# Kernel optimization log

Measured on AMD Instinct MI355X. Metric: run time of the kernel, lower is better.

The kernel has to match this reference:

```python
import jax, jax.numpy as jnp
import numpy as np

B, N, E = 4, 2048, 1024
A, H = 64, 16          # attention_feature_dim, heads
D = A                   # per-head dim per source's rearrange quirk: d = attention_feature_dim
DK = A / H              # source scales by sqrt(attention_feature_dim / heads) = sqrt(4)
NEG_INF = jnp.float32(-jnp.inf)


def setup_inputs() -> dict:
    key = jax.random.key(0)
    ks = jax.random.split(key, 6)
    x = jax.random.normal(ks[0], (B, N, E), dtype=jnp.float32)
    mask = jax.random.randint(ks[1], (B, N), 0, 2, dtype=jnp.int32)
    # nn.Linear(E, A*H*3): weight [out,in] -> store transposed [in,out] for x @ W
    w_qkv = jax.random.normal(ks[2], (E, A * H * 3), dtype=jnp.float32) / np.sqrt(E)
    b_qkv = jax.random.normal(ks[3], (A * H * 3,), dtype=jnp.float32) * 0.02
    w_out = jax.random.normal(ks[4], (A * H, E), dtype=jnp.float32) / np.sqrt(A * H)
    b_out = jax.random.normal(ks[5], (E,), dtype=jnp.float32) * 0.02
    return {"x": x, "mask": mask, "w_qkv": w_qkv, "b_qkv": b_qkv,
            "w_out": w_out, "b_out": b_out}


def reference(x, mask, w_qkv, b_qkv, w_out, b_out):
    b, n, _ = x.shape
    qkv = x @ w_qkv + b_qkv                         # [b, n, 3*H*D]
    q, k, v = jnp.split(qkv, 3, axis=-1)            # each [b, n, H*D]
    def to_heads(t):
        return t.reshape(b, n, H, D).transpose(0, 2, 1, 3)  # [b, H, n, D]
    q, k, v = to_heads(q), to_heads(k), to_heads(v)
    scale = jnp.float32(1.0 / np.sqrt(DK))
    scores = jnp.einsum('bhqd,bhkd->bhqk', q, k) * scale    # [b, H, n, n]
    # mask: [b, n] -> [b, 1, 1, n]; masked positions (==0) get -inf
    scores = jnp.where(mask[:, None, None, :] == 0, NEG_INF, scores)
    attn = jax.nn.softmax(scores, axis=-1)
    out = jnp.einsum('bhqk,bhkd->bhqd', attn, v)            # [b, H, n, D]
    out = out.transpose(0, 2, 1, 3).reshape(b, n, H * D)    # [b, n, H*D]
    return out @ w_out + b_out                              # [b, n, E]
```

## Files before the change

kernel.cpp:

```cpp
#include <hip/hip_runtime.h>


typedef __bf16 bf16;
typedef __attribute__((ext_vector_type(8))) __bf16 bf16x8;
typedef __attribute__((ext_vector_type(4))) float f32x4;

#define MFMA16(a, b, c) __builtin_amdgcn_mfma_f32_16x16x32_bf16(a, b, c, 0, 0, 0)
#define GLOAD_LDS(src, dst) __builtin_amdgcn_global_load_lds( \
    (const __attribute__((address_space(1))) void*)(src),     \
    (__attribute__((address_space(3))) void*)(dst), 16, 0, 0)
#define BAR() __builtin_amdgcn_s_barrier()
#define VMCNT(n) asm volatile("s_waitcnt vmcnt(" #n ")" ::: "memory")

#define QSCALE 0.72134752f

__device__ __forceinline__ void transpose_tile(
    const float* __restrict__ in, bf16* __restrict__ out, int R, int C,
    int scale_rows, float scale, int bx, int by, int t, float (*s)[65])
{
    const int r0 = by * 64;
    const int c0 = bx * 64;
    const int tr  = t >> 4;
    const int tc4 = (t & 15) * 4;
#pragma unroll
    for (int p = 0; p < 4; ++p) {
        int r = tr + p * 16;
        float4 v = *(const float4*)(in + (size_t)(r0 + r) * C + c0 + tc4);
        s[r][tc4 + 0] = v.x; s[r][tc4 + 1] = v.y;
        s[r][tc4 + 2] = v.z; s[r][tc4 + 3] = v.w;
    }
    __syncthreads();
    const int cw  = t >> 3;
    const int rw8 = (t & 7) * 8;
#pragma unroll
    for (int p = 0; p < 2; ++p) {
        int c = cw + p * 32;
        float f = (c0 + c) < scale_rows ? scale : 1.0f;
        union { uint4 v; bf16 h[8]; } u;
#pragma unroll
        for (int j = 0; j < 8; ++j) u.h[j] = (bf16)(s[rw8 + j][c] * f);
        *(uint4*)(out + (size_t)(c0 + c) * R + r0 + rw8) = u.v;
    }
}

__global__ __launch_bounds__(256, 1) void prep_kernel(
    const float* __restrict__ x, bf16* __restrict__ xb,
    const float* __restrict__ w_qkv, bf16* __restrict__ wqkvT,
    const float* __restrict__ w_out, bf16* __restrict__ woutT)
{
    __shared__ float s[64][65];
    const int t = threadIdx.x;
    int blk = blockIdx.x;
    if (blk < 8192) {
        int i = blk * 256 + t;
        float4 v = *(const float4*)(x + (size_t)i * 4);
        union { ushort4 u; bf16 h[4]; } o;
        o.h[0] = (bf16)v.x; o.h[1] = (bf16)v.y;
        o.h[2] = (bf16)v.z; o.h[3] = (bf16)v.w;
        *(ushort4*)(xb + (size_t)i * 4) = o.u;
        return;
    }
    blk -= 8192;
    if (blk < 768) {
        transpose_tile(w_qkv, wqkvT, 1024, 3072, 1024, QSCALE,
                       blk % 48, blk / 48, t, s);
    } else {
        blk -= 768;
        transpose_tile(w_out, woutT, 1024, 1024, 0, 1.0f,
                       blk % 16, blk / 16, t, s);
    }
}

template <typename OutT>
__global__ __launch_bounds__(512, 2) void gemm128x256_kernel(
    const bf16* __restrict__ A, const bf16* __restrict__ Bt,
    const float* __restrict__ bias, OutT* __restrict__ C,
    int M, int ldc, int K, int qcols, float qscale, int nbx,
    bf16* __restrict__ vtg)
{
    __shared__ __align__(16) bf16 As[3 * 128 * 64];
    __shared__ __align__(16) bf16 Bs[3 * 256 * 64];

    const int t    = threadIdx.x;
    const int lane = t & 63;
    const int wave = t >> 6;
    const int wr   = wave >> 2;
    const int wc   = wave & 3;
    const int l15  = lane & 15;
    const int g    = lane >> 4;

    const int nwg  = gridDim.x;
    const int per  = nwg >> 3;
    const int mper = per / nbx;
    const int wg   = blockIdx.x;
    const int xcd  = wg & 7;
    const int idx  = wg >> 3;
    const int m0   = (xcd * mper + idx % mper) * 128;
    const int n0   = (idx / mper) * 256;

    const int ntile = K >> 6;

    int srow[2], sblk[2];
#pragma unroll
    for (int r = 0; r < 2; ++r) {
        int s = t * 16 + r * 8192;
        srow[r] = s >> 7;
        int blk = (s >> 4) & 7;
        sblk[r] = blk ^ (srow[r] & 7);
    }
    const int ldst0 = t * 8;

    const bf16* Abase = A  + (size_t)m0 * K;
    const bf16* Bbase = Bt + (size_t)n0 * K;

    const f32x4 z = {0.f, 0.f, 0.f, 0.f};
    f32x4 acc[4][4];
#pragma unroll
    for (int i = 0; i < 4; ++i)
#pragma unroll
        for (int j = 0; j < 4; ++j) acc[i][j] = z;

    auto stageA = [&](int tile, int slot) {
        if (tile >= ntile) return;
        bf16* dst = As + slot * 8192;
        const bf16* src = Abase + tile * 64;
#pragma unroll
        for (int r = 0; r < 2; ++r)
            GLOAD_LDS(src + (size_t)srow[r] * K + sblk[r] * 8,
                      dst + ldst0 + r * 4096);
    };
    auto stageBh = [&](int tile, int slot, int h) {
        if (tile >= ntile) return;
        bf16* dst = Bs + slot * 16384 + h * 8192;
        const bf16* src = Bbase + (size_t)(h * 128) * K + tile * 64;
#pragma unroll
        for (int r = 0; r < 2; ++r)
            GLOAD_LDS(src + (size_t)srow[r] * K + sblk[r] * 8,
                      dst + ldst0 + r * 4096);
    };

#define LOAD_AF(slot)                                                         \
    _Pragma("unroll")                                                         \
    for (int f = 0; f < 4; ++f) {                                             \
        int row = wr * 64 + f * 16 + l15;                                     \
        _Pragma("unroll")                                                     \
        for (int ks = 0; ks < 2; ++ks)                                        \
            af[f][ks] = *(const bf16x8*)(&As[(slot) * 8192 + row * 64 +       \
                            (((ks * 4 + g) ^ (row & 7)) * 8)]);               \
    }
#define LOAD_BF(slot, half, dstv)                                             \
    _Pragma("unroll")                                                         \
    for (int c2 = 0; c2 < 2; ++c2) {                                          \
        int row = wc * 64 + ((half) * 2 + c2) * 16 + l15;                     \
        _Pragma("unroll")                                                     \
        for (int ks = 0; ks < 2; ++ks)                                        \
            dstv[c2][ks] = *(const bf16x8*)(&Bs[(slot) * 16384 + row * 64 +   \
                            (((ks * 4 + g) ^ (row & 7)) * 8)]);               \
    }
#define MFMA_H(bv, half)                                                      \
    {                                                                         \
        __builtin_amdgcn_s_setprio(1);                                        \
        _Pragma("unroll")                                                     \
        for (int f = 0; f < 4; ++f)                                           \
            _Pragma("unroll")                                                 \
            for (int c2 = 0; c2 < 2; ++c2) {                                  \
                acc[f][(half) * 2 + c2] = MFMA16(                             \
                    af[f][0], bv[c2][0], acc[f][(half) * 2 + c2]);            \
                acc[f][(half) * 2 + c2] = MFMA16(                             \
                    af[f][1], bv[c2][1], acc[f][(half) * 2 + c2]);            \
            }                                                                 \
        __builtin_amdgcn_s_setprio(0);                                        \
    }

    stageA(0, 0); stageBh(0, 0, 0); stageBh(0, 0, 1);
    stageA(1, 1); stageBh(1, 1, 0); stageBh(1, 1, 1);
    VMCNT(6);
    BAR();

    int slot = 0;
    for (int T = 0; T < ntile; ++T) {
        int slot2 = slot + 2; if (slot2 >= 3) slot2 -= 3;
        bf16x8 af[4][2], blo[2][2], bhi[2][2];
        LOAD_AF(slot);
        LOAD_BF(slot, 0, blo);
        stageA(T + 2, slot2);
        stageBh(T + 2, slot2, 0);
        MFMA_H(blo, 0);
        BAR();
        LOAD_BF(slot, 1, bhi);
        stageBh(T + 2, slot2, 1);
        MFMA_H(bhi, 1);
        if (T + 1 < ntile) {
            if (T + 2 < ntile) { VMCNT(6); } else { VMCNT(0); }
        }
        BAR();
        slot = (slot == 2) ? 0 : slot + 1;
    }

#undef LOAD_AF
#undef LOAD_BF
#undef MFMA_H

    if (vtg != nullptr && n0 >= 2048) {
        const int b = m0 >> 11;
#pragma unroll
        for (int f = 0; f < 4; ++f) {
            int row = m0 + wr * 64 + f * 16 + g * 4;
            int n   = row & 2047;
#pragma unroll
            for (int cf = 0; cf < 4; ++cf) {
                int col = n0 + wc * 64 + cf * 16 + l15;
                int c2  = col - 2048;
                int h   = c2 >> 6;
                int d   = c2 & 63;
                float bs = bias[col];
                union { bf16 hh[4]; ushort4 u; } s;
#pragma unroll
                for (int r = 0; r < 4; ++r)
                    s.hh[r] = (bf16)(acc[f][cf][r] + bs);
                *(ushort4*)(vtg + (size_t)(b * 16 + h) * 131072 +
                            (size_t)d * 2048 + n) = s.u;
            }
        }
    } else {
#pragma unroll
        for (int f = 0; f < 4; ++f) {
            int row = m0 + wr * 64 + f * 16 + g * 4;
#pragma unroll
            for (int cf = 0; cf < 4; ++cf) {
                int col = n0 + wc * 64 + cf * 16 + l15;
                float bs = bias[col];
                if (col < qcols) bs *= qscale;
#pragma unroll
                for (int r = 0; r < 4; ++r) {
                    float v = acc[f][cf][r] + bs;
                    C[(size_t)(row + r) * ldc + col] = (OutT)v;
                }
            }
        }
    }
}

__global__ __launch_bounds__(256, 3) void attn_kernel(
    const bf16* __restrict__ qkv, const bf16* __restrict__ vtg,
    const int* __restrict__ mask, bf16* __restrict__ O)
{
    __shared__ __align__(16) bf16 Ks[2][64 * 64];
    __shared__ __align__(16) bf16 Vt[2][64 * 64];
    __shared__ __align__(16) bf16 Ps[4][16 * 88];
    __shared__ __align__(16) float mneg[2048];

    const int t    = threadIdx.x;
    const int lane = t & 63;
    const int wave = t >> 6;
    const int l15  = lane & 15;
    const int g    = lane >> 4;

    const int bid = (blockIdx.x & 7) * 128 + (blockIdx.x >> 3);
    const int qt  = bid & 15;
    const int bh  = bid >> 4;
    const int h   = bh & 15;
    const int b   = bh >> 4;
    const int q0  = qt * 128 + wave * 16;

    const int* mrow = mask + b * 2048;
    for (int i = t; i < 2048; i += 256)
        mneg[i] = mrow[i] ? 0.0f : -1e30f;

    const size_t RS = 2048;
    const bf16* qp0 = qkv + (size_t)(b * 2048 + q0 + l15) * RS + h * 64 + g * 8;
    const bf16* qp1 = qp0 + (size_t)64 * RS;
    bf16x8 aQ[2][2];
    aQ[0][0] = *(const bf16x8*)(qp0);
    aQ[0][1] = *(const bf16x8*)(qp0 + 32);
    aQ[1][0] = *(const bf16x8*)(qp1);
    aQ[1][1] = *(const bf16x8*)(qp1 + 32);

    const bf16* kbase = qkv + (size_t)(b * 2048) * RS + 1024 + h * 64;
    const bf16* vbase = vtg + (size_t)bh * (64 * 2048);

    const int e0 = t * 8;
    int srow[2], scol[2];
#pragma unroll
    for (int r = 0; r < 2; ++r) {
        int e   = e0 + r * 2048;
        int row = e >> 6;
        int cb  = (e >> 3) & 7;
        srow[r] = row;
        scol[r] = ((cb ^ (row & 7)) * 8);
    }

    const int rb0 = ((g)     ^ (l15 & 7)) * 8;
    const int rb1 = ((4 + g) ^ (l15 & 7)) * 8;

    const f32x4 z = {0.f, 0.f, 0.f, 0.f};
    f32x4 o0[4] = {z, z, z, z}, o1[4] = {z, z, z, z};
    f32x4 lacc0 = z, lacc1 = z;

    bf16x8 ones;
#pragma unroll
    for (int j = 0; j < 8; ++j) ones[j] = (bf16)1.0f;

#pragma unroll
    for (int r = 0; r < 2; ++r) {
        GLOAD_LDS(kbase + (size_t)srow[r] * RS + scol[r],   &Ks[0][e0 + r * 2048]);
        GLOAD_LDS(vbase + (size_t)srow[r] * 2048 + scol[r], &Vt[0][e0 + r * 2048]);
    }
    asm volatile("s_waitcnt vmcnt(0)" ::: "memory");
    __syncthreads();

    for (int i = 0; i < 32; ++i) {
        const int kc  = i * 64;
        const int buf = i & 1;

        if (i + 1 < 32) {
#pragma unroll
            for (int r = 0; r < 2; ++r) {
                GLOAD_LDS(kbase + (size_t)(kc + 64 + srow[r]) * RS + scol[r],
                          &Ks[buf ^ 1][e0 + r * 2048]);
                GLOAD_LDS(vbase + (size_t)srow[r] * 2048 + kc + 64 + scol[r],
                          &Vt[buf ^ 1][e0 + r * 2048]);
            }
        }

        f32x4 mb4[4];
#pragma unroll
        for (int kt = 0; kt < 4; ++kt)
#pragma unroll
            for (int r = 0; r < 4; ++r)
                mb4[kt][r] = mneg[kc + kt * 16 + g * 4 + r];

        bf16x8 bk[4][2];
#pragma unroll
        for (int kt = 0; kt < 4; ++kt) {
            const bf16* kr = &Ks[buf][(kt * 16 + l15) * 64];
            bk[kt][0] = *(const bf16x8*)(kr + rb0);
            bk[kt][1] = *(const bf16x8*)(kr + rb1);
        }

        f32x4 S[4];
#pragma unroll
        for (int kt = 0; kt < 4; ++kt) {
            S[kt] = MFMA16(bk[kt][0], aQ[0][0], mb4[kt]);
            S[kt] = MFMA16(bk[kt][1], aQ[0][1], S[kt]);
        }
#pragma unroll
        for (int kt = 0; kt < 4; ++kt) {
            union { bf16 hh[4]; ushort4 u; } pk;
#pragma unroll
            for (int r = 0; r < 4; ++r)
                pk.hh[r] = (bf16)__builtin_amdgcn_exp2f(S[kt][r]);
            *(ushort4*)(&Ps[wave][l15 * 88 + kt * 16 + g * 4]) = pk.u;
        }
        asm volatile("s_waitcnt lgkmcnt(0)" ::: "memory");
        __builtin_amdgcn_sched_barrier(0);
        const bf16x8 aP00 = *(const bf16x8*)(&Ps[wave][l15 * 88 + g * 8]);
        const bf16x8 aP01 = *(const bf16x8*)(&Ps[wave][l15 * 88 + 32 + g * 8]);
        asm volatile("s_waitcnt lgkmcnt(0)" ::: "memory");
        __builtin_amdgcn_sched_barrier(0);

#pragma unroll
        for (int kt = 0; kt < 4; ++kt) {
            S[kt] = MFMA16(bk[kt][0], aQ[1][0], mb4[kt]);
            S[kt] = MFMA16(bk[kt][1], aQ[1][1], S[kt]);
        }

        bf16x8 bv[4][2];
#pragma unroll
        for (int dt = 0; dt < 4; ++dt) {
            const bf16* vr = &Vt[buf][(dt * 16 + l15) * 64];
            bv[dt][0] = *(const bf16x8*)(vr + rb0);
            bv[dt][1] = *(const bf16x8*)(vr + rb1);
        }

#pragma unroll
        for (int kt = 0; kt < 4; ++kt) {
            union { bf16 hh[4]; ushort4 u; } pk;
#pragma unroll
            for (int r = 0; r < 4; ++r)
                pk.hh[r] = (bf16)__builtin_amdgcn_exp2f(S[kt][r]);
            *(ushort4*)(&Ps[wave][l15 * 88 + kt * 16 + g * 4]) = pk.u;
        }

        lacc0 = MFMA16(aP00, ones, lacc0);
        lacc0 = MFMA16(aP01, ones, lacc0);
#pragma unroll
        for (int dt = 0; dt < 4; ++dt) {
            o0[dt] = MFMA16(aP00, bv[dt][0], o0[dt]);
            o0[dt] = MFMA16(aP01, bv[dt][1], o0[dt]);
        }
        asm volatile("s_waitcnt lgkmcnt(0)" ::: "memory");
        __builtin_amdgcn_sched_barrier(0);
        const bf16x8 aP10 = *(const bf16x8*)(&Ps[wave][l15 * 88 + g * 8]);
        const bf16x8 aP11 = *(const bf16x8*)(&Ps[wave][l15 * 88 + 32 + g * 8]);

        lacc1 = MFMA16(aP10, ones, lacc1);
        lacc1 = MFMA16(aP11, ones, lacc1);
#pragma unroll
        for (int dt = 0; dt < 4; ++dt) {
            o1[dt] = MFMA16(aP10, bv[dt][0], o1[dt]);
            o1[dt] = MFMA16(aP11, bv[dt][1], o1[dt]);
        }

        asm volatile("s_waitcnt vmcnt(0)" ::: "memory");
        __syncthreads();
    }

    float inv0[4], inv1[4];
#pragma unroll
    for (int r = 0; r < 4; ++r) {
        inv0[r] = 1.0f / fmaxf(lacc0[r], 1e-30f);
        inv1[r] = 1.0f / fmaxf(lacc1[r], 1e-30f);
    }
#pragma unroll
    for (int nt = 0; nt < 4; ++nt) {
#pragma unroll
        for (int r = 0; r < 4; ++r) {
            int d = nt * 16 + l15;
            int row0 = q0 + g * 4 + r;
            O[(size_t)(b * 2048 + row0) * 1024 + h * 64 + d] = (bf16)(o0[nt][r] * inv0[r]);
            O[(size_t)(b * 2048 + row0 + 64) * 1024 + h * 64 + d] = (bf16)(o1[nt][r] * inv1[r]);
        }
    }
}

extern "C" void kernel_launch(void* const* d_in, const int* in_sizes, int n_in,
                              void* d_out, int out_size, void* d_ws, size_t ws_size,
                              hipStream_t stream)
{
    const float* x     = (const float*)d_in[0];
    const int*   mask  = (const int*)d_in[1];
    const float* w_qkv = (const float*)d_in[2];
    const float* b_qkv = (const float*)d_in[3];
    const float* w_out = (const float*)d_in[4];
    const float* b_out = (const float*)d_in[5];
    float* out = (float*)d_out;

    char* ws = (char*)d_ws;
    bf16* qkvb  = (bf16*)(ws);
    bf16* Obuf  = (bf16*)(ws + 33554432);
    bf16* xb    = (bf16*)(ws + 50331648);
    bf16* wqkvT = (bf16*)(ws + 67108864);
    bf16* woutT = (bf16*)(ws + 73400320);
    bf16* vtg   = (bf16*)(ws + 75497472);

    prep_kernel<<<dim3(9216), 256, 0, stream>>>(x, xb, w_qkv, wqkvT, w_out, woutT);
    gemm128x256_kernel<bf16><<<dim3(768), 512, 0, stream>>>(
        xb, wqkvT, b_qkv, qkvb, 8192, 2048, 1024, 1024, QSCALE, 12, vtg);
    attn_kernel<<<dim3(1024), 256, 0, stream>>>(qkvb, vtg, mask, Obuf);
    gemm128x256_kernel<float><<<dim3(256), 512, 0, stream>>>(
        Obuf, woutT, b_out, out, 8192, 1024, 1024, 0, 1.0f, 4, nullptr);
}
```

Measured before the change: 274.8 us.

## Keep softmax probabilities in registers via transposed MFMA and permuted V layout

Computes S with K as the A operand so exp'd probabilities land in registers already laid out as the B operand for the PV MFMA. This removes the per-wave LDS round trip (Ps buffer, stores, waitcnts and reloads). The V^T store in the QKV GEMM epilogue permutes the key index within 32-blocks so it matches the register order, and O is accumulated transposed with vectorized ushort4 output stores. It depends on the permutation being exactly consistent between producer and consumer, and it frees LDS, which may raise occupancy.

After: 251.2 us. -8.6%, faster.

```diff
diff --git a/kernel.cpp b/kernel.cpp
--- a/kernel.cpp
+++ b/kernel.cpp
@@ -207,6 +207,9 @@
         for (int f = 0; f < 4; ++f) {
             int row = m0 + wr * 64 + f * 16 + g * 4;
             int n   = row & 2047;
+            int k   = n & 31;
+            int pos = (k < 16) ? ((k >> 2) * 8) : (((k - 16) >> 2) * 8 + 4);
+            int np  = (n & ~31) + pos;
 #pragma unroll
             for (int cf = 0; cf < 4; ++cf) {
                 int col = n0 + wc * 64 + cf * 16 + l15;
@@ -219,7 +222,7 @@
                 for (int r = 0; r < 4; ++r)
                     s.hh[r] = (bf16)(acc[f][cf][r] + bs);
                 *(ushort4*)(vtg + (size_t)(b * 16 + h) * 131072 +
-                            (size_t)d * 2048 + n) = s.u;
+                            (size_t)d * 2048 + np) = s.u;
             }
         }
     } else {
@@ -247,7 +250,6 @@
 {
     __shared__ __align__(16) bf16 Ks[2][64 * 64];
     __shared__ __align__(16) bf16 Vt[2][64 * 64];
-    __shared__ __align__(16) bf16 Ps[4][16 * 88];
     __shared__ __align__(16) float mneg[2048];
 
     const int t    = threadIdx.x;
@@ -292,6 +294,8 @@
 
     const int rb0 = ((g)     ^ (l15 & 7)) * 8;
     const int rb1 = ((4 + g) ^ (l15 & 7)) * 8;
+    const int vb0 = ((g)     ^ (l15 & 7)) * 8;
+    const int vb1 = ((4 + g) ^ (l15 & 7)) * 8;
 
     const f32x4 z = {0.f, 0.f, 0.f, 0.f};
     f32x4 o0[4] = {z, z, z, z}, o1[4] = {z, z, z, z};
@@ -338,89 +342,64 @@
             bk[kt][1] = *(const bf16x8*)(kr + rb1);
         }
 
-        f32x4 S[4];
+        f32x4 S0[4], S1[4];
 #pragma unroll
         for (int kt = 0; kt < 4; ++kt) {
-            S[kt] = MFMA16(bk[kt][0], aQ[0][0], mb4[kt]);
-            S[kt] = MFMA16(bk[kt][1], aQ[0][1], S[kt]);
-        }
-#pragma unroll
-        for (int kt = 0; kt < 4; ++kt) {
-            union { bf16 hh[4]; ushort4 u; } pk;
-#pragma unroll
-            for (int r = 0; r < 4; ++r)
-                pk.hh[r] = (bf16)__builtin_amdgcn_exp2f(S[kt][r]);
-            *(ushort4*)(&Ps[wave][l15 * 88 + kt * 16 + g * 4]) = pk.u;
-        }
-        asm volatile("s_waitcnt lgkmcnt(0)" ::: "memory");
-        __builtin_amdgcn_sched_barrier(0);
-        const bf16x8 aP00 = *(const bf16x8*)(&Ps[wave][l15 * 88 + g * 8]);
-        const bf16x8 aP01 = *(const bf16x8*)(&Ps[wave][l15 * 88 + 32 + g * 8]);
-        asm volatile("s_waitcnt lgkmcnt(0)" ::: "memory");
-        __builtin_amdgcn_sched_barrier(0);
-
-#pragma unroll
-        for (int kt = 0; kt < 4; ++kt) {
-            S[kt] = MFMA16(bk[kt][0], aQ[1][0], mb4[kt]);
-            S[kt] = MFMA16(bk[kt][1], aQ[1][1], S[kt]);
-        }
-
-        bf16x8 bv[4][2];
+            S0[kt] = MFMA16(bk[kt][0], aQ[0][0], mb4[kt]);
+            S0[kt] = MFMA16(bk[kt][1], aQ[0][1], S0[kt]);
+            S1[kt] = MFMA16(bk[kt][0], aQ[1][0], mb4[kt]);
+            S1[kt] = MFMA16(bk[kt][1], aQ[1][1], S1[kt]);
+        }
+
+        bf16x8 pb0[2], pb1[2];
+#pragma unroll
+        for (int m = 0; m < 2; ++m) {
+            union { bf16 hh[8]; bf16x8 v; } u0, u1;
+#pragma unroll
+            for (int j = 0; j < 4; ++j) {
+                u0.hh[j]     = (bf16)__builtin_amdgcn_exp2f(S0[2 * m][j]);
+                u0.hh[4 + j] = (bf16)__builtin_amdgcn_exp2f(S0[2 * m + 1][j]);
+                u1.hh[j]     = (bf16)__builtin_amdgcn_exp2f(S1[2 * m][j]);
+                u1.hh[4 + j] = (bf16)__builtin_amdgcn_exp2f(S1[2 * m + 1][j]);
+            }
+            pb0[m] = u0.v;
+            pb1[m] = u1.v;
+        }
+
+        lacc0 = MFMA16(ones, pb0[0], lacc0);
+        lacc0 = MFMA16(ones, pb0[1], lacc0);
+        lacc1 = MFMA16(ones, pb1[0], lacc1);
+        lacc1 = MFMA16(ones, pb1[1], lacc1);
+
 #pragma unroll
         for (int dt = 0; dt < 4; ++dt) {
             const bf16* vr = &Vt[buf][(dt * 16 + l15) * 64];
-            bv[dt][0] = *(const bf16x8*)(vr + rb0);
-            bv[dt][1] = *(const bf16x8*)(vr + rb1);
-        }
-
-#pragma unroll
-        for (int kt = 0; kt < 4; ++kt) {
-            union { bf16 hh[4]; ushort4 u; } pk;
-#pragma unroll
-            for (int r = 0; r < 4; ++r)
-                pk.hh[r] = (bf16)__builtin_amdgcn_exp2f(S[kt][r]);
-            *(ushort4*)(&Ps[wave][l15 * 88 + kt * 16 + g * 4]) = pk.u;
-        }
-
-        lacc0 = MFMA16(aP00, ones, lacc0);
-        lacc0 = MFMA16(aP01, ones, lacc0);
-#pragma unroll
-        for (int dt = 0; dt < 4; ++dt) {
-            o0[dt] = MFMA16(aP00, bv[dt][0], o0[dt]);
-            o0[dt] = MFMA16(aP01, bv[dt][1], o0[dt]);
-        }
-        asm volatile("s_waitcnt lgkmcnt(0)" ::: "memory");
-        __builtin_amdgcn_sched_barrier(0);
-        const bf16x8 aP10 = *(const bf16x8*)(&Ps[wave][l15 * 88 + g * 8]);
-        const bf16x8 aP11 = *(const bf16x8*)(&Ps[wave][l15 * 88 + 32 + g * 8]);
-
-        lacc1 = MFMA16(aP10, ones, lacc1);
-        lacc1 = MFMA16(aP11, ones, lacc1);
-#pragma unroll
-        for (int dt = 0; dt < 4; ++dt) {
-            o1[dt] = MFMA16(aP10, bv[dt][0], o1[dt]);
-            o1[dt] = MFMA16(aP11, bv[dt][1], o1[dt]);
+            bf16x8 vv0 = *(const bf16x8*)(vr + vb0);
+            bf16x8 vv1 = *(const bf16x8*)(vr + vb1);
+            o0[dt] = MFMA16(vv0, pb0[0], o0[dt]);
+            o0[dt] = MFMA16(vv1, pb0[1], o0[dt]);
+            o1[dt] = MFMA16(vv0, pb1[0], o1[dt]);
+            o1[dt] = MFMA16(vv1, pb1[1], o1[dt]);
         }
 
         asm volatile("s_waitcnt vmcnt(0)" ::: "memory");
         __syncthreads();
     }
 
-    float inv0[4], inv1[4];
-#pragma unroll
-    for (int r = 0; r < 4; ++r) {
-        inv0[r] = 1.0f / fmaxf(lacc0[r], 1e-30f);
-        inv1[r] = 1.0f / fmaxf(lacc1[r], 1e-30f);
-    }
-#pragma unroll
-    for (int nt = 0; nt < 4; ++nt) {
+    const float inv0 = 1.0f / fmaxf(lacc0[0], 1e-30f);
+    const float inv1 = 1.0f / fmaxf(lacc1[0], 1e-30f);
+    bf16* op0 = O + (size_t)(b * 2048 + q0 + l15) * 1024 + h * 64 + g * 4;
+    bf16* op1 = op0 + (size_t)64 * 1024;
+#pragma unroll
+    for (int dt = 0; dt < 4; ++dt) {
+        union { bf16 hh[4]; ushort4 u; } s0, s1;
 #pragma unroll
         for (int r = 0; r < 4; ++r) {
-            int d = nt * 16 + l15;
-            int row0 = q0 + g * 4 + r;
-            O[(size_t)(b * 2048 + row0) * 1024 + h * 64 + d] = (bf16)(o0[nt][r] * inv0[r]);
-            O[(size_t)(b * 2048 + row0 + 64) * 1024 + h * 64 + d] = (bf16)(o1[nt][r] * inv1[r]);
-        }
+            s0.hh[r] = (bf16)(o0[dt][r] * inv0);
+            s1.hh[r] = (bf16)(o1[dt][r] * inv1);
+        }
+        *(ushort4*)(op0 + dt * 16) = s0.u;
+        *(ushort4*)(op1 + dt * 16) = s1.u;
     }
 }
 
```
